# Performance work log

Measured on AMD Instinct MI355X. Metric: run time of the kernel, lower is better.

The kernel has to match this reference:

```python
import jax, jax.numpy as jnp
from jax import lax
import numpy as np

B_SZ, L, D_MODEL, N_STATE, K_CONV, D_RANK = 2, 1024, 768, 16, 4, 48
DT_MIN, DT_MAX = 1e-4, 0.1


def setup_inputs() -> dict:
    key = jax.random.key(0)
    ks = jax.random.split(key, 8)
    s = 0.02
    x = jax.random.normal(ks[0], (B_SZ, L, D_MODEL), jnp.float32)
    W_in = jax.random.normal(ks[1], (D_MODEL, 2 * D_MODEL), jnp.float32) * s
    conv_w = jax.random.normal(ks[2], (D_MODEL, 1, K_CONV), jnp.float32) * 0.2
    conv_b = jnp.zeros((D_MODEL,), jnp.float32)
    W_x = jax.random.normal(ks[3], (D_MODEL, D_RANK + 2 * N_STATE), jnp.float32) * s
    W_delta = jax.random.normal(ks[4], (D_RANK, D_MODEL), jnp.float32) * s
    b_delta = jnp.zeros((D_MODEL,), jnp.float32)
    # Mamba S4D-real init: A_log = log(1..N) repeated over D
    A_log = jnp.log(jnp.tile(jnp.arange(1, N_STATE + 1, dtype=jnp.float32)[None, :], (D_MODEL, 1)))
    D_param = jnp.ones((D_MODEL,), jnp.float32)
    W_out = jax.random.normal(ks[5], (D_MODEL, D_MODEL), jnp.float32) * s
    return dict(x=x, W_in=W_in, conv_w=conv_w, conv_b=conv_b, W_x=W_x,
                W_delta=W_delta, b_delta=b_delta, A_log=A_log, D_param=D_param, W_out=W_out)


def _selective_scan(u, delta, A, Bm, Cm, Dp):
    # u, delta: (B,L,D); A: (D,N); Bm,Cm: (B,L,N); Dp: (D,)
    dA = jnp.einsum('bld,dn->bldn', delta, A)            # (B,L,D,N)
    dB_u = jnp.einsum('bld,bld,bln->bldn', delta, u, Bm)  # (B,L,D,N)
    # tf.pad(dA[:,1:],[[0,0],[1,1],...])[:,1:] == shift left by one, zero at end
    shifted = jnp.concatenate([dA[:, 1:], jnp.zeros_like(dA[:, :1])], axis=1)
    cs = jnp.flip(jnp.cumsum(jnp.flip(shifted, axis=1), axis=1), axis=1)
    dA_cs = jnp.exp(cs)
    xs = jnp.cumsum(dB_u * dA_cs, axis=1) / (dA_cs + 1e-12)
    y = jnp.einsum('bldn,bln->bld', xs, Cm)
    return y + u * Dp


def reference(x, W_in, conv_w, conv_b, W_x, W_delta, b_delta, A_log, D_param, W_out):
    Bb, Ll, Dm = x.shape
    Kk = conv_w.shape[-1]
    xr = x @ W_in                                   # (B,L,2D)
    xs, res = jnp.split(xr, 2, axis=-1)
    # depthwise causal conv over L (channels_first, groups=D)
    xc = jnp.transpose(xs, (0, 2, 1))               # (B,D,L)
    xc = lax.conv_general_dilated(xc, conv_w, window_strides=(1,),
                                  padding=[(Kk - 1, 0)],
                                  dimension_numbers=('NCL', 'OIL', 'NCL'),
                                  feature_group_count=Dm)
    xc = xc + conv_b[None, :, None]
    xs = jax.nn.silu(jnp.transpose(xc, (0, 2, 1)))  # (B,L,D)
    # SSM parameterization
    A = -jnp.exp(A_log)                             # (D,N)
    xp = xs @ W_x                                   # (B,L,dr+2N)
    dr = W_delta.shape[0]
    Nn = A_log.shape[1]
    delta, Bm, Cm = jnp.split(xp, [dr, dr + Nn], axis=-1)
    delta = jax.nn.softplus(delta @ W_delta + b_delta)
    delta = jnp.clip(delta, DT_MIN, DT_MAX)
    y = _selective_scan(xs, delta, A, Bm, Cm, D_param)
    y = y * jax.nn.silu(res)
    return y @ W_out
```

## Files before the change

kernel.cpp:

```cpp
#include <hip/hip_runtime.h>
#include <math.h>

#define LSEQ 1024
#define DM   768
#define NS   16
#define DR   48
#define BSZ  2
#define R2   (BSZ*LSEQ)
#define NC   128
#define LC   (LSEQ/NC)
#define KSP  6

typedef __bf16 bf16x2 __attribute__((ext_vector_type(2)));
typedef __bf16 bf16x4 __attribute__((ext_vector_type(4)));
typedef __bf16 bf16x8 __attribute__((ext_vector_type(8)));
typedef float  f32x4  __attribute__((ext_vector_type(4)));

template<int ABF16, int OUTBF16, int EPI>
__global__ __launch_bounds__(256) void gemm_t64(const void* __restrict__ Av,
                                                const float* __restrict__ B,
                                                void* __restrict__ Cv,
                                                void* __restrict__ C1v,
                                                const float* __restrict__ bias,
                                                int K, int Ksrc, int lda, int ldb, int ldc,
                                                int split) {
    __shared__ __align__(16) __bf16 As[64][40];
    __shared__ __align__(16) __bf16 Bs[64][40];
    const int tid  = threadIdx.x;
    const int lane = tid & 63;
    const int wave = tid >> 6;
    const int r = lane & 15, q = lane >> 4;
    const int n0 = blockIdx.x * 64, m0 = blockIdx.y * 64;

    const int arow = tid >> 2, ak8 = (tid & 3) * 8;
    const int nq = tid & 15, kg = (tid >> 4) & 7;

    f32x4 zero = {0.f, 0.f, 0.f, 0.f};
    f32x4 acc[4];
    #pragma unroll
    for (int nt = 0; nt < 4; ++nt) acc[nt] = zero;

    f32x4 a0, a1, b_pf[4];
    bf16x8 a8;
    if (ABF16) {
        const __bf16* A = (const __bf16*)Av;
        a8 = *(const bf16x8*)(A + (size_t)(m0 + arow) * lda + ak8);
    } else {
        const float* A = (const float*)Av;
        a0 = (ak8     < Ksrc) ? *(const f32x4*)(A + (size_t)(m0 + arow) * lda + ak8)     : zero;
        a1 = (ak8 + 4 < Ksrc) ? *(const f32x4*)(A + (size_t)(m0 + arow) * lda + ak8 + 4) : zero;
    }
    if (tid < 128) {
        #pragma unroll
        for (int i = 0; i < 4; ++i) {
            int k = kg * 4 + i;
            b_pf[i] = (k < Ksrc) ? *(const f32x4*)(B + (size_t)k * ldb + n0 + nq * 4) : zero;
        }
    }

    const int KT = K / 32;
    for (int kt = 0; kt < KT; ++kt) {
        if (ABF16) {
            *(bf16x8*)&As[arow][ak8] = a8;
        } else {
            bf16x4 p0 = {(__bf16)a0[0], (__bf16)a0[1], (__bf16)a0[2], (__bf16)a0[3]};
            bf16x4 p1 = {(__bf16)a1[0], (__bf16)a1[1], (__bf16)a1[2], (__bf16)a1[3]};
            *(bf16x4*)&As[arow][ak8]     = p0;
            *(bf16x4*)&As[arow][ak8 + 4] = p1;
        }
        if (tid < 128) {
            #pragma unroll
            for (int c = 0; c < 4; ++c) {
                bf16x4 pk = {(__bf16)b_pf[0][c], (__bf16)b_pf[1][c],
                             (__bf16)b_pf[2][c], (__bf16)b_pf[3][c]};
                *(bf16x4*)&Bs[nq * 4 + c][kg * 4] = pk;
            }
        }
        __syncthreads();
        if (kt + 1 < KT) {
            int k0 = (kt + 1) * 32;
            if (ABF16) {
                const __bf16* A = (const __bf16*)Av;
                a8 = *(const bf16x8*)(A + (size_t)(m0 + arow) * lda + k0 + ak8);
            } else {
                const float* A = (const float*)Av;
                a0 = (k0 + ak8     < Ksrc)
                     ? *(const f32x4*)(A + (size_t)(m0 + arow) * lda + k0 + ak8)     : zero;
                a1 = (k0 + ak8 + 4 < Ksrc)
                     ? *(const f32x4*)(A + (size_t)(m0 + arow) * lda + k0 + ak8 + 4) : zero;
            }
            if (tid < 128) {
                #pragma unroll
                for (int i = 0; i < 4; ++i) {
                    int k = k0 + kg * 4 + i;
                    b_pf[i] = (k < Ksrc) ? *(const f32x4*)(B + (size_t)k * ldb + n0 + nq * 4)
                                         : zero;
                }
            }
        }
        bf16x8 af = *(const bf16x8*)&As[wave * 16 + r][q * 8];
        #pragma unroll
        for (int nt = 0; nt < 4; ++nt) {
            bf16x8 bfr = *(const bf16x8*)&Bs[nt * 16 + r][q * 8];
            acc[nt] = __builtin_amdgcn_mfma_f32_16x16x32_bf16(af, bfr, acc[nt], 0, 0, 0);
        }
        __syncthreads();
    }
    const int rowb = m0 + wave * 16 + q * 4;
    void* Cd = Cv;
    int nbase = n0;
    if (EPI == 1 && n0 >= split) { Cd = C1v; nbase = n0 - split; }
    #pragma unroll
    for (int nt = 0; nt < 4; ++nt) {
        int col = nbase + nt * 16 + r;
        float bcol = (EPI == 2) ? bias[n0 + nt * 16 + r] : 0.f;
        #pragma unroll
        for (int rr = 0; rr < 4; ++rr) {
            float z = acc[nt][rr];
            if (EPI == 2) {
                z += bcol;
                z = (z > 20.f) ? z : log1pf(expf(z));
                z = fminf(fmaxf(z, 1e-4f), 0.1f);
            }
            if (OUTBF16)
                ((__bf16*)Cd)[(size_t)(rowb + rr) * ldc + col] = (__bf16)z;
            else
                ((float*)Cd)[(size_t)(rowb + rr) * ldc + col] = z;
        }
    }
}

__global__ __launch_bounds__(256) void conv_silu_b(const __bf16* __restrict__ xs,
                                                   const float* __restrict__ cw,
                                                   const float* __restrict__ cb,
                                                   __bf16* __restrict__ u) {
    const int idx = blockIdx.x * 256 + threadIdx.x;
    const int r  = idx / (DM / 2);
    const int dh = idx - r * (DM / 2);
    const int d  = dh * 2;
    const int l  = r & (LSEQ - 1);
    f32x4 w0 = *(const f32x4*)(cw + d * 4);
    f32x4 w1 = *(const f32x4*)(cw + d * 4 + 4);
    float a0 = cb[d], a1 = cb[d + 1];
    #pragma unroll
    for (int k = 0; k < 4; ++k) {
        if (l - 3 + k >= 0) {
            bf16x2 v = *(const bf16x2*)(xs + (size_t)(r - 3 + k) * DM + d);
            a0 += (float)v[0] * w0[k];
            a1 += (float)v[1] * w1[k];
        }
    }
    float u0 = a0 / (1.f + expf(-a0));
    float u1 = a1 / (1.f + expf(-a1));
    bf16x2 o = {(__bf16)u0, (__bf16)u1};
    *(bf16x2*)(u + (size_t)r * DM + d) = o;
}

__global__ __launch_bounds__(256) void gemm_wx_sk(const __bf16* __restrict__ U,
                                                  const float* __restrict__ Wx,
                                                  float* __restrict__ xpp) {
    __shared__ __align__(16) __bf16 As2[64][40];
    __shared__ __align__(16) __bf16 Ws[80][40];
    const int tid  = threadIdx.x;
    const int lane = tid & 63;
    const int wave = tid >> 6;
    const int r = lane & 15, q = lane >> 4;
    const int m0 = blockIdx.x * 64;
    const int kbase = blockIdx.y * (768 / KSP);
    const int arow = tid >> 2, ak8 = (tid & 3) * 8;
    const int nq = tid % 20, kq = tid / 20;

    f32x4 acc[5];
    #pragma unroll
    for (int nt = 0; nt < 5; ++nt) acc[nt] = {0.f, 0.f, 0.f, 0.f};

    bf16x8 a_pf;
    f32x4 w_pf[4];
    a_pf = *(const bf16x8*)(U + (size_t)(m0 + arow) * DM + kbase + ak8);
    if (tid < 160) {
        #pragma unroll
        for (int i = 0; i < 4; ++i)
            w_pf[i] = *(const f32x4*)(Wx + (size_t)(kbase + kq * 4 + i) * 80 + nq * 4);
    }

    const int KT = (768 / KSP) / 32;
    for (int kt = 0; kt < KT; ++kt) {
        *(bf16x8*)&As2[arow][ak8] = a_pf;
        if (tid < 160) {
            #pragma unroll
            for (int c = 0; c < 4; ++c) {
                bf16x4 pk = {(__bf16)w_pf[0][c], (__bf16)w_pf[1][c],
                             (__bf16)w_pf[2][c], (__bf16)w_pf[3][c]};
                *(bf16x4*)&Ws[nq * 4 + c][kq * 4] = pk;
            }
        }
        __syncthreads();
        if (kt + 1 < KT) {
            int k0 = kbase + (kt + 1) * 32;
            a_pf = *(const bf16x8*)(U + (size_t)(m0 + arow) * DM + k0 + ak8);
            if (tid < 160) {
                #pragma unroll
                for (int i = 0; i < 4; ++i)
                    w_pf[i] = *(const f32x4*)(Wx + (size_t)(k0 + kq * 4 + i) * 80 + nq * 4);
            }
        }
        bf16x8 af = *(const bf16x8*)&As2[wave * 16 + r][q * 8];
        #pragma unroll
        for (int nt = 0; nt < 5; ++nt) {
            bf16x8 bfr = *(const bf16x8*)&Ws[nt * 16 + r][q * 8];
            acc[nt] = __builtin_amdgcn_mfma_f32_16x16x32_bf16(af, bfr, acc[nt], 0, 0, 0);
        }
        __syncthreads();
    }
    #pragma unroll
    for (int nt = 0; nt < 5; ++nt) {
        int col  = nt * 16 + r;
        int rowb = m0 + wave * 16 + q * 4;
        #pragma unroll
        for (int rr = 0; rr < 4; ++rr)
            xpp[((size_t)blockIdx.y * R2 + rowb + rr) * 80 + col] = acc[nt][rr];
    }
}

__global__ __launch_bounds__(256) void reduce_xp(const float* __restrict__ xpp,
                                                 float* __restrict__ xp) {
    const size_t i = ((size_t)blockIdx.x * 256 + threadIdx.x) * 4;
    f32x4 s = *(const f32x4*)(xpp + i);
    #pragma unroll
    for (int k = 1; k < KSP; ++k) {
        f32x4 v = *(const f32x4*)(xpp + (size_t)k * R2 * 80 + i);
        s[0] += v[0]; s[1] += v[1]; s[2] += v[2]; s[3] += v[3];
    }
    *(f32x4*)(xp + i) = s;
}

__global__ __launch_bounds__(128) void scan_part1(const __bf16* __restrict__ delta,
                                                  const __bf16* __restrict__ u,
                                                  const float* __restrict__ xp,
                                                  const float* __restrict__ A_log,
                                                  float* __restrict__ Eprod,
                                                  float* __restrict__ Hend,
                                                  float* __restrict__ SDel) {
    __shared__ float sB[LC][NS];
    const int tid = threadIdx.x;
    const int blk = blockIdx.x;
    const int ch = blk % NC;
    const int dg = (blk / NC) % (DM / 128);
    const int b  = blk / (NC * (DM / 128));
    const int d  = dg * 128 + tid;
    const int l0 = ch * LC;
    const int bd = b * DM + d;

    for (int i = tid; i < LC * NS; i += 128) {
        int l = i >> 4, n = i & 15;
        sB[l][n] = xp[(size_t)(b * LSEQ + l0 + l) * 80 + DR + n];
    }
    float c[NS];
    #pragma unroll
    for (int n = 0; n < NS; ++n) c[n] = -__expf(A_log[d * NS + n]);
    __syncthreads();

    float h[NS], ep[NS];
    #pragma unroll
    for (int n = 0; n < NS; ++n) { h[n] = 0.f; ep[n] = 1.f; }
    float pd = 0.f;
    for (int l = 0; l < LC; ++l) {
        size_t rr = (size_t)(b * LSEQ + l0 + l);
        float dlt = (float)delta[rr * DM + d];
        float uu  = (float)u[rr * DM + d];
        pd += dlt;
        float du = dlt * uu;
        #pragma unroll
        for (int n = 0; n < NS; ++n) {
            float e = __expf(c[n] * dlt);
            h[n]  = e * h[n] + du * sB[l][n];
            ep[n] *= e;
        }
    }
    #pragma unroll
    for (int n = 0; n < NS; ++n) {
        size_t idx = ((size_t)ch * NS + n) * (BSZ * DM) + bd;
        Eprod[idx] = ep[n];
        Hend[idx]  = h[n];
    }
    SDel[(size_t)ch * (BSZ * DM) + bd] = pd;
}

__global__ __launch_bounds__(256) void scan_combine(const float* __restrict__ Eprod,
                                                    float* __restrict__ Hend,
                                                    float* __restrict__ SDel,
                                                    float* __restrict__ TD) {
    const int t = blockIdx.x * 256 + threadIdx.x;
    const int BD = BSZ * DM;
    float H = 0.f;
    for (int cg = 0; cg < NC; cg += 8) {
        float e[8], he[8];
        #pragma unroll
        for (int j = 0; j < 8; ++j) {
            size_t idx = (size_t)(cg + j) * (NS * BD) + t;
            e[j]  = Eprod[idx];
            he[j] = Hend[idx];
        }
        #pragma unroll
        for (int j = 0; j < 8; ++j) {
            size_t idx = (size_t)(cg + j) * (NS * BD) + t;
            Hend[idx] = H;
            H = e[j] * H + he[j];
        }
    }
    if (t < BD) {
        float pd = 0.f;
        for (int cg = 0; cg < NC; cg += 8) {
            float s[8];
            #pragma unroll
            for (int j = 0; j < 8; ++j) s[j] = SDel[(size_t)(cg + j) * BD + t];
            #pragma unroll
            for (int j = 0; j < 8; ++j) {
                SDel[(size_t)(cg + j) * BD + t] = pd;
                pd += s[j];
            }
        }
        TD[t] = pd;
    }
}

__global__ __launch_bounds__(128) void scan_part3(const __bf16* __restrict__ delta,
                                                  const __bf16* __restrict__ u,
                                                  const float* __restrict__ xp,
                                                  const __bf16* __restrict__ res,
                                                  const float* __restrict__ A_log,
                                                  const float* __restrict__ Dp,
                                                  const float* __restrict__ Hin,
                                                  const float* __restrict__ PD0,
                                                  const float* __restrict__ TD,
                                                  __bf16* __restrict__ g) {
    __shared__ float sB[LC][NS];
    __shared__ float sC[LC][NS];
    const int tid = threadIdx.x;
    const int blk = blockIdx.x;
    const int ch = blk % NC;
    const int dg = (blk / NC) % (DM / 128);
    const int b  = blk / (NC * (DM / 128));
    const int d  = dg * 128 + tid;
    const int l0 = ch * LC;
    const int bd = b * DM + d;

    for (int i = tid; i < LC * NS; i += 128) {
        int l = i >> 4, n = i & 15;
        size_t rr = (size_t)(b * LSEQ + l0 + l) * 80;
        sB[l][n] = xp[rr + DR + n];
        sC[l][n] = xp[rr + DR + NS + n];
    }
    float c[NS], h[NS];
    #pragma unroll
    for (int n = 0; n < NS; ++n) {
        c[n] = -__expf(A_log[d * NS + n]);
        h[n] = Hin[((size_t)ch * NS + n) * (BSZ * DM) + bd];
    }
    float pd = PD0[(size_t)ch * (BSZ * DM) + bd];
    const float td = TD[bd];
    const float dp = Dp[d];
    __syncthreads();

    for (int l = 0; l < LC; ++l) {
        size_t rr = (size_t)(b * LSEQ + l0 + l);
        float dlt = (float)delta[rr * DM + d];
        float uu  = (float)u[rr * DM + d];
        float rv  = (float)res[rr * DM + d];
        pd += dlt;
        float du = dlt * uu;
        float x = td - pd;
        float y = 0.f;
        #pragma unroll
        for (int n = 0; n < NS; ++n) {
            float e = __expf(c[n] * dlt);
            h[n] = e * h[n] + du * sB[l][n];
            float P = __expf(-c[n] * x);
            float den = 1.0f + 1e-12f * P;
            y += h[n] * sC[l][n] * __builtin_amdgcn_rcpf(den);
        }
        y += uu * dp;
        float sig = __builtin_amdgcn_rcpf(1.f + __expf(-rv));
        g[rr * DM + d] = (__bf16)(y * rv * sig);
    }
}

extern "C" void kernel_launch(void* const* d_in, const int* in_sizes, int n_in,
                              void* d_out, int out_size, void* d_ws, size_t ws_size,
                              hipStream_t stream) {
    const float* x       = (const float*)d_in[0];
    const float* W_in    = (const float*)d_in[1];
    const float* conv_w  = (const float*)d_in[2];
    const float* conv_b  = (const float*)d_in[3];
    const float* W_x     = (const float*)d_in[4];
    const float* W_delta = (const float*)d_in[5];
    const float* b_delta = (const float*)d_in[6];
    const float* A_log   = (const float*)d_in[7];
    const float* D_param = (const float*)d_in[8];
    const float* W_out   = (const float*)d_in[9];
    float* out = (float*)d_out;

    char* p = (char*)d_ws;
    __bf16* xs    = (__bf16*)p;  p += (size_t)R2 * DM * 2;
    __bf16* res   = (__bf16*)p;  p += (size_t)R2 * DM * 2;
    __bf16* u     = (__bf16*)p;  p += (size_t)R2 * DM * 2;
    float*  xp    = (float*)p;   p += (size_t)R2 * 80 * 4;
    __bf16* delta = (__bf16*)p;  p += (size_t)R2 * DM * 2;
    float*  xpp   = (float*)p;   p += (size_t)KSP * R2 * 80 * 4;
    float*  Eprod = (float*)p;   p += (size_t)NC * NS * BSZ * DM * 4;
    float*  Hend  = (float*)p;   p += (size_t)NC * NS * BSZ * DM * 4;
    float*  SDel  = (float*)p;   p += (size_t)NC * BSZ * DM * 4;
    float*  TD    = (float*)p;
    __bf16* g     = u;

    gemm_t64<0, 1, 1><<<dim3(1536 / 64, R2 / 64), 256, 0, stream>>>(
        x, W_in, xs, res, nullptr, 768, 768, 768, 1536, 768, 768);
    conv_silu_b<<<(R2 * DM / 2) / 256, 256, 0, stream>>>(xs, conv_w, conv_b, u);
    gemm_wx_sk<<<dim3(R2 / 64, KSP), 256, 0, stream>>>(u, W_x, xpp);
    reduce_xp<<<(R2 * 80 / 4) / 256, 256, 0, stream>>>(xpp, xp);
    gemm_t64<0, 1, 2><<<dim3(DM / 64, R2 / 64), 256, 0, stream>>>(
        xp, W_delta, delta, delta, b_delta, 64, 48, 80, 768, 768, 1 << 30);
    scan_part1<<<BSZ * (DM / 128) * NC, 128, 0, stream>>>(delta, u, xp, A_log,
                                                          Eprod, Hend, SDel);
    scan_combine<<<(NS * BSZ * DM) / 256, 256, 0, stream>>>(Eprod, Hend, SDel, TD);
    scan_part3<<<BSZ * (DM / 128) * NC, 128, 0, stream>>>(delta, u, xp, res, A_log, D_param,
                                                          Hend, SDel, TD, g);
    gemm_t64<1, 0, 0><<<dim3(DM / 64, R2 / 64), 256, 0, stream>>>(
        g, W_out, out, out, nullptr, 768, 768, 768, 768, 768, 1 << 30);
}
```

Before: 188.6 us.

## Fuse split-K xp reduction into consumers, halve scan chunks, shrink combine blocks

Removes the separate reduce_xp kernel and lets the delta GEMM and both scan kernels sum the KSP split-K partial buffers directly as they load xp. This drops one launch and one write/read pass over xp, but consumers now read the partials several times over. The chunk count for the chunked scan drops from 128 to 64, which gives longer sequential chunks and fewer partial states to combine. scan_combine moves to 64-thread blocks so it launches more blocks.

```diff
diff --git a/kernel.cpp b/kernel.cpp
--- a/kernel.cpp
+++ b/kernel.cpp
@@ -7,16 +7,17 @@
 #define DR   48
 #define BSZ  2
 #define R2   (BSZ*LSEQ)
-#define NC   128
+#define NC   64
 #define LC   (LSEQ/NC)
 #define KSP  6
+#define XPR  (R2*80)
 
 typedef __bf16 bf16x2 __attribute__((ext_vector_type(2)));
 typedef __bf16 bf16x4 __attribute__((ext_vector_type(4)));
 typedef __bf16 bf16x8 __attribute__((ext_vector_type(8)));
 typedef float  f32x4  __attribute__((ext_vector_type(4)));
 
-template<int ABF16, int OUTBF16, int EPI>
+template<int ABF16, int OUTBF16, int EPI, int ASUM>
 __global__ __launch_bounds__(256) void gemm_t64(const void* __restrict__ Av,
                                                 const float* __restrict__ B,
                                                 void* __restrict__ Cv,
@@ -42,21 +43,47 @@
 
     f32x4 a0, a1, b_pf[4];
     bf16x8 a8;
-    if (ABF16) {
-        const __bf16* A = (const __bf16*)Av;
-        a8 = *(const bf16x8*)(A + (size_t)(m0 + arow) * lda + ak8);
-    } else {
-        const float* A = (const float*)Av;
-        a0 = (ak8     < Ksrc) ? *(const f32x4*)(A + (size_t)(m0 + arow) * lda + ak8)     : zero;
-        a1 = (ak8 + 4 < Ksrc) ? *(const f32x4*)(A + (size_t)(m0 + arow) * lda + ak8 + 4) : zero;
-    }
-    if (tid < 128) {
+    auto loadA = [&](int kbase) {
+        if (ABF16) {
+            const __bf16* A = (const __bf16*)Av;
+            a8 = *(const bf16x8*)(A + (size_t)(m0 + arow) * lda + kbase + ak8);
+        } else if (ASUM > 0) {
+            const float* A = (const float*)Av;
+            a0 = zero; a1 = zero;
+            if (kbase + ak8 < Ksrc) {
+                #pragma unroll
+                for (int s2 = 0; s2 < ASUM; ++s2) {
+                    f32x4 v = *(const f32x4*)(A + (size_t)s2 * XPR
+                                              + (size_t)(m0 + arow) * lda + kbase + ak8);
+                    a0[0] += v[0]; a0[1] += v[1]; a0[2] += v[2]; a0[3] += v[3];
+                }
+            }
+            if (kbase + ak8 + 4 < Ksrc) {
+                #pragma unroll
+                for (int s2 = 0; s2 < ASUM; ++s2) {
+                    f32x4 v = *(const f32x4*)(A + (size_t)s2 * XPR
+                                              + (size_t)(m0 + arow) * lda + kbase + ak8 + 4);
+                    a1[0] += v[0]; a1[1] += v[1]; a1[2] += v[2]; a1[3] += v[3];
+                }
+            }
+        } else {
+            const float* A = (const float*)Av;
+            a0 = (kbase + ak8     < Ksrc)
+                 ? *(const f32x4*)(A + (size_t)(m0 + arow) * lda + kbase + ak8)     : zero;
+            a1 = (kbase + ak8 + 4 < Ksrc)
+                 ? *(const f32x4*)(A + (size_t)(m0 + arow) * lda + kbase + ak8 + 4) : zero;
+        }
+    };
+    auto loadB = [&](int kbase) {
         #pragma unroll
         for (int i = 0; i < 4; ++i) {
-            int k = kg * 4 + i;
+            int k = kbase + kg * 4 + i;
             b_pf[i] = (k < Ksrc) ? *(const f32x4*)(B + (size_t)k * ldb + n0 + nq * 4) : zero;
         }
-    }
+    };
+
+    loadA(0);
+    if (tid < 128) loadB(0);
 
     const int KT = K / 32;
     for (int kt = 0; kt < KT; ++kt) {
@@ -78,25 +105,8 @@
         }
         __syncthreads();
         if (kt + 1 < KT) {
-            int k0 = (kt + 1) * 32;
-            if (ABF16) {
-                const __bf16* A = (const __bf16*)Av;
-                a8 = *(const bf16x8*)(A + (size_t)(m0 + arow) * lda + k0 + ak8);
-            } else {
-                const float* A = (const float*)Av;
-                a0 = (k0 + ak8     < Ksrc)
-                     ? *(const f32x4*)(A + (size_t)(m0 + arow) * lda + k0 + ak8)     : zero;
-                a1 = (k0 + ak8 + 4 < Ksrc)
-                     ? *(const f32x4*)(A + (size_t)(m0 + arow) * lda + k0 + ak8 + 4) : zero;
-            }
-            if (tid < 128) {
-                #pragma unroll
-                for (int i = 0; i < 4; ++i) {
-                    int k = k0 + kg * 4 + i;
-                    b_pf[i] = (k < Ksrc) ? *(const f32x4*)(B + (size_t)k * ldb + n0 + nq * 4)
-                                         : zero;
-                }
-            }
+            loadA((kt + 1) * 32);
+            if (tid < 128) loadB((kt + 1) * 32);
         }
         bf16x8 af = *(const bf16x8*)&As[wave * 16 + r][q * 8];
         #pragma unroll
@@ -218,25 +228,13 @@
         int rowb = m0 + wave * 16 + q * 4;
         #pragma unroll
         for (int rr = 0; rr < 4; ++rr)
-            xpp[((size_t)blockIdx.y * R2 + rowb + rr) * 80 + col] = acc[nt][rr];
-    }
-}
-
-__global__ __launch_bounds__(256) void reduce_xp(const float* __restrict__ xpp,
-                                                 float* __restrict__ xp) {
-    const size_t i = ((size_t)blockIdx.x * 256 + threadIdx.x) * 4;
-    f32x4 s = *(const f32x4*)(xpp + i);
-    #pragma unroll
-    for (int k = 1; k < KSP; ++k) {
-        f32x4 v = *(const f32x4*)(xpp + (size_t)k * R2 * 80 + i);
-        s[0] += v[0]; s[1] += v[1]; s[2] += v[2]; s[3] += v[3];
-    }
-    *(f32x4*)(xp + i) = s;
+            xpp[((size_t)blockIdx.y * XPR + (size_t)(rowb + rr) * 80 + col)] = acc[nt][rr];
+    }
 }
 
 __global__ __launch_bounds__(128) void scan_part1(const __bf16* __restrict__ delta,
                                                   const __bf16* __restrict__ u,
-                                                  const float* __restrict__ xp,
+                                                  const float* __restrict__ xpp,
                                                   const float* __restrict__ A_log,
                                                   float* __restrict__ Eprod,
                                                   float* __restrict__ Hend,
@@ -253,7 +251,11 @@
 
     for (int i = tid; i < LC * NS; i += 128) {
         int l = i >> 4, n = i & 15;
-        sB[l][n] = xp[(size_t)(b * LSEQ + l0 + l) * 80 + DR + n];
+        size_t off = (size_t)(b * LSEQ + l0 + l) * 80 + DR + n;
+        float s = 0.f;
+        #pragma unroll
+        for (int ks = 0; ks < KSP; ++ks) s += xpp[(size_t)ks * XPR + off];
+        sB[l][n] = s;
     }
     float c[NS];
     #pragma unroll
@@ -286,11 +288,11 @@
     SDel[(size_t)ch * (BSZ * DM) + bd] = pd;
 }
 
-__global__ __launch_bounds__(256) void scan_combine(const float* __restrict__ Eprod,
-                                                    float* __restrict__ Hend,
-                                                    float* __restrict__ SDel,
-                                                    float* __restrict__ TD) {
-    const int t = blockIdx.x * 256 + threadIdx.x;
+__global__ __launch_bounds__(64) void scan_combine(const float* __restrict__ Eprod,
+                                                   float* __restrict__ Hend,
+                                                   float* __restrict__ SDel,
+                                                   float* __restrict__ TD) {
+    const int t = blockIdx.x * 64 + threadIdx.x;
     const int BD = BSZ * DM;
     float H = 0.f;
     for (int cg = 0; cg < NC; cg += 8) {
@@ -326,7 +328,7 @@
 
 __global__ __launch_bounds__(128) void scan_part3(const __bf16* __restrict__ delta,
                                                   const __bf16* __restrict__ u,
-                                                  const float* __restrict__ xp,
+                                                  const float* __restrict__ xpp,
                                                   const __bf16* __restrict__ res,
                                                   const float* __restrict__ A_log,
                                                   const float* __restrict__ Dp,
@@ -347,9 +349,15 @@
 
     for (int i = tid; i < LC * NS; i += 128) {
         int l = i >> 4, n = i & 15;
-        size_t rr = (size_t)(b * LSEQ + l0 + l) * 80;
-        sB[l][n] = xp[rr + DR + n];
-        sC[l][n] = xp[rr + DR + NS + n];
+        size_t offB = (size_t)(b * LSEQ + l0 + l) * 80 + DR + n;
+        float sb = 0.f, sc = 0.f;
+        #pragma unroll
+        for (int ks = 0; ks < KSP; ++ks) {
+            sb += xpp[(size_t)ks * XPR + offB];
+            sc += xpp[(size_t)ks * XPR + offB + NS];
+        }
+        sB[l][n] = sb;
+        sC[l][n] = sc;
     }
     float c[NS], h[NS];
     #pragma unroll
@@ -404,27 +412,25 @@
     __bf16* xs    = (__bf16*)p;  p += (size_t)R2 * DM * 2;
     __bf16* res   = (__bf16*)p;  p += (size_t)R2 * DM * 2;
     __bf16* u     = (__bf16*)p;  p += (size_t)R2 * DM * 2;
-    float*  xp    = (float*)p;   p += (size_t)R2 * 80 * 4;
     __bf16* delta = (__bf16*)p;  p += (size_t)R2 * DM * 2;
-    float*  xpp   = (float*)p;   p += (size_t)KSP * R2 * 80 * 4;
+    float*  xpp   = (float*)p;   p += (size_t)KSP * XPR * 4;
     float*  Eprod = (float*)p;   p += (size_t)NC * NS * BSZ * DM * 4;
     float*  Hend  = (float*)p;   p += (size_t)NC * NS * BSZ * DM * 4;
     float*  SDel  = (float*)p;   p += (size_t)NC * BSZ * DM * 4;
     float*  TD    = (float*)p;
     __bf16* g     = u;
 
-    gemm_t64<0, 1, 1><<<dim3(1536 / 64, R2 / 64), 256, 0, stream>>>(
+    gemm_t64<0, 1, 1, 0><<<dim3(1536 / 64, R2 / 64), 256, 0, stream>>>(
         x, W_in, xs, res, nullptr, 768, 768, 768, 1536, 768, 768);
     conv_silu_b<<<(R2 * DM / 2) / 256, 256, 0, stream>>>(xs, conv_w, conv_b, u);
     gemm_wx_sk<<<dim3(R2 / 64, KSP), 256, 0, stream>>>(u, W_x, xpp);
-    reduce_xp<<<(R2 * 80 / 4) / 256, 256, 0, stream>>>(xpp, xp);
-    gemm_t64<0, 1, 2><<<dim3(DM / 64, R2 / 64), 256, 0, stream>>>(
-        xp, W_delta, delta, delta, b_delta, 64, 48, 80, 768, 768, 1 << 30);
-    scan_part1<<<BSZ * (DM / 128) * NC, 128, 0, stream>>>(delta, u, xp, A_log,
+    gemm_t64<0, 1, 2, KSP><<<dim3(DM / 64, R2 / 64), 256, 0, stream>>>(
+        xpp, W_delta, delta, delta, b_delta, 64, 48, 80, 768, 768, 1 << 30);
+    scan_part1<<<BSZ * (DM / 128) * NC, 128, 0, stream>>>(delta, u, xpp, A_log,
                                                           Eprod, Hend, SDel);
-    scan_combine<<<(NS * BSZ * DM) / 256, 256, 0, stream>>>(Eprod, Hend, SDel, TD);
-    scan_part3<<<BSZ * (DM / 128) * NC, 128, 0, stream>>>(delta, u, xp, res, A_log, D_param,
+    scan_combine<<<(NS * BSZ * DM) / 64, 64, 0, stream>>>(Eprod, Hend, SDel, TD);
+    scan_part3<<<BSZ * (DM / 128) * NC, 128, 0, stream>>>(delta, u, xpp, res, A_log, D_param,
                                                           Hend, SDel, TD, g);
-    gemm_t64<1, 0, 0><<<dim3(DM / 64, R2 / 64), 256, 0, stream>>>(
+    gemm_t64<1, 0, 0, 0><<<dim3(DM / 64, R2 / 64), 256, 0, stream>>>(
         g, W_out, out, out, nullptr, 768, 768, 768, 768, 768, 1 << 30);
 }
```

New measurement: 186.5 us. No clear change (-1.1%).
